# Performance work log

Hardware: AMD Instinct MI355X
Metric: run time of the kernel (lower is better)

## Reference

```python
import jax, jax.numpy as jnp
import numpy as np

N_NODES = 100000


def setup_inputs() -> dict:
    key = jax.random.key(0)
    k1, k2, k3 = jax.random.split(key, 3)
    x = jax.random.normal(k1, (N_NODES, 128), dtype=jnp.float32)
    # Flattened hyperedge membership: src_idx = member node ids, dst_idx = target
    # node id of the owning hyperedge (repeated once per member).
    src_idx = jax.random.randint(k2, (2000000,), 0, N_NODES, dtype=jnp.int64)
    dst_idx = jax.random.randint(k3, (2000000,), 0, N_NODES, dtype=jnp.int64)
    return {"x": x, "src_idx": src_idx, "dst_idx": dst_idx}


def reference(x, src_idx, dst_idx):
    # Gather member features, aggregate per target node, add residual.
    # (The torch identity-stack weight matmul is exactly a per-hyperedge sum,
    #  which the flattened scatter_add reproduces.)
    x_j = x[src_idx]                                        # [E_total, d]
    agg = jax.ops.segment_sum(x_j, dst_idx, num_segments=x.shape[0])  # [N, d]
    return x + agg
```

## Files before the change

kernel.cpp:

```cpp
#include <hip/hip_runtime.h>
#include <hip/hip_fp16.h>


constexpr int DIM = 128;
constexpr int BSHIFT = 7;
constexpr int GNODES = 1 << BSHIFT;
constexpr int MAXB = 1024;
constexpr int CE = 8192;
constexpr int CAP_MAX = 3072;
constexpr int QCAP = 1536;
constexpr int CONVCH = 8192;

__global__ void hgnn_fused_prep(const float4* __restrict__ x4,
                                ushort4* __restrict__ xh4, int n4,
                                const int* __restrict__ src,
                                const int* __restrict__ dst,
                                int* __restrict__ cursor,
                                int* __restrict__ arena, int cap,
                                int* __restrict__ spillCnt,
                                int2* __restrict__ spill, int spillCap,
                                int* __restrict__ qctr, int nChunks,
                                int nedges, int nbk, int nPart) {
    __shared__ int h[MAXB];
    __shared__ int lb[MAXB];
    __shared__ int chunkS;
    const int tid = threadIdx.x;

    if ((int)blockIdx.x < nPart) {
        int c0 = blockIdx.x * CE;
        int c1 = min(c0 + CE, nedges);
        for (int i = tid; i < nbk; i += blockDim.x) h[i] = 0;
        __syncthreads();
        for (int i = c0 + tid; i < c1; i += blockDim.x)
            atomicAdd(&h[dst[i] >> BSHIFT], 1);
        __syncthreads();
        for (int i = tid; i < nbk; i += blockDim.x)
            lb[i] = h[i] ? atomicAdd(&cursor[i], h[i]) : 0;
        __syncthreads();
        for (int i = c0 + tid; i < c1; i += blockDim.x) {
            int s = src[i];
            int d = dst[i];
            int bk = d >> BSHIFT;
            int pos = atomicAdd(&lb[bk], 1);
            if (pos < cap) {
                arena[(size_t)bk * cap + pos] = s | ((d & (GNODES - 1)) << 17);
            } else {
                int sp = atomicAdd(spillCnt, 1);
                if (sp < spillCap) spill[sp] = make_int2(s, d);
            }
        }
    } else if ((int)blockIdx.x == nPart) {
        if (tid < 32) {
            ushort4 z; z.x = 0; z.y = 0; z.z = 0; z.w = 0;
            xh4[n4 + tid] = z;
        }
    }

    for (;;) {
        if (tid == 0) chunkS = atomicAdd(qctr, 1);
        __syncthreads();
        int chunk = chunkS;
        __syncthreads();
        if (chunk >= nChunks) break;
        int i0 = chunk * CONVCH;
        int i1 = min(i0 + CONVCH, n4);
        for (int i = i0 + tid; i < i1; i += blockDim.x) {
            float4 v = x4[i];
            ushort4 o;
            o.x = __half_as_ushort(__float2half_rn(v.x));
            o.y = __half_as_ushort(__float2half_rn(v.y));
            o.z = __half_as_ushort(__float2half_rn(v.z));
            o.w = __half_as_ushort(__float2half_rn(v.w));
            xh4[i] = o;
        }
    }
}

__global__ void hgnn_aggregate(const float4* __restrict__ x4,
                               const uint2* __restrict__ xh,
                               const int* __restrict__ arena, int cap,
                               const int* __restrict__ cursor,
                               float4* __restrict__ out4, int nnodes,
                               int* __restrict__ spillCnt,
                               int2* __restrict__ spill, int spillCap) {
    __shared__ int qsorted[QCAP];
    __shared__ int hoff[33];
    __shared__ int hcur[32];

    const int b = blockIdx.x >> 2;
    const int q = blockIdx.x & 3;
    const int tid = threadIdx.x;
    const int wv = tid >> 6;
    const int lane = tid & 63;
    const int h = lane >> 5;
    const int c = lane & 31;
    const int ZROW = nnodes;

    int cnt = cursor[b];
    if (cnt > cap) cnt = cap;
    const int* ar = arena + (size_t)b * cap;

    if (tid < 32) hcur[tid] = 0;
    __syncthreads();
    for (int i = tid; i < cnt; i += blockDim.x) {
        int dl = ar[i] >> 17;
        if ((dl >> 5) == q) atomicAdd(&hcur[dl & 31], 1);
    }
    __syncthreads();

    int myc = (tid < 32) ? hcur[tid] : 0;
    if (tid < 32) hoff[tid + 1] = myc;
    if (tid == 0) hoff[0] = 0;
    __syncthreads();
    for (int off = 1; off < 32; off <<= 1) {
        int v = (tid < 32 && tid >= off) ? hoff[tid + 1 - off] : 0;
        __syncthreads();
        if (tid < 32) hoff[tid + 1] += v;
        __syncthreads();
    }
    if (tid < 32) hcur[tid] = hoff[tid];
    __syncthreads();

    for (int i = tid; i < cnt; i += blockDim.x) {
        int p = ar[i];
        int dl = p >> 17;
        if ((dl >> 5) == q) {
            int pos = atomicAdd(&hcur[dl & 31], 1);
            if (pos < QCAP) {
                qsorted[pos] = p;
            } else {
                int sp = atomicAdd(spillCnt, 1);
                if (sp < spillCap)
                    spill[sp] = make_int2(p & 0x1FFFF, (b << BSHIFT) + dl);
            }
        }
    }
    __syncthreads();

    const int nodeBase = (b << BSHIFT) + q * 32 + wv * 8;
    const __half2 hz = __floats2half2_rn(0.f, 0.f);
    for (int r = 0; r < 8; r += 2) {
        int n0 = nodeBase + r;
        if (n0 >= nnodes) break;
        int n1 = n0 + 1;
        bool has1 = n1 < nnodes;

        int bin0 = wv * 8 + r;
        int s0 = hoff[bin0];
        int e0 = hoff[bin0 + 1];
        int s1 = hoff[bin0 + 1];
        int e1 = hoff[bin0 + 2];
        if (s0 > QCAP) s0 = QCAP;
        if (e0 > QCAP) e0 = QCAP;
        if (s1 > QCAP) s1 = QCAP;
        if (e1 > QCAP) e1 = QCAP;
        int m0 = e0 - s0;
        int m1 = has1 ? (e1 - s1) : 0;
        int mm = max(m0, m1);

        __half2 a0lo = hz, a0hi = hz, b0lo = hz, b0hi = hz;
        __half2 a1lo = hz, a1hi = hz, b1lo = hz, b1hi = hz;

        for (int j = 0; j < mm; j += 16) {
#pragma unroll
            for (int k = 0; k < 8; ++k) {
                int e = j + 2 * k + h;
                int p0 = (e < m0) ? (qsorted[s0 + e] & 0x1FFFF) : ZROW;
                int p1 = (e < m1) ? (qsorted[s1 + e] & 0x1FFFF) : ZROW;
                uint2 v0 = xh[(size_t)p0 * 32 + c];
                uint2 v1 = xh[(size_t)p1 * 32 + c];
                __half2 v0lo = *reinterpret_cast<const __half2*>(&v0.x);
                __half2 v0hi = *reinterpret_cast<const __half2*>(&v0.y);
                __half2 v1lo = *reinterpret_cast<const __half2*>(&v1.x);
                __half2 v1hi = *reinterpret_cast<const __half2*>(&v1.y);
                if (k & 1) {
                    b0lo = __hadd2(b0lo, v0lo); b0hi = __hadd2(b0hi, v0hi);
                    b1lo = __hadd2(b1lo, v1lo); b1hi = __hadd2(b1hi, v1hi);
                } else {
                    a0lo = __hadd2(a0lo, v0lo); a0hi = __hadd2(a0hi, v0hi);
                    a1lo = __hadd2(a1lo, v1lo); a1hi = __hadd2(a1hi, v1hi);
                }
            }
        }

        {
            __half2 slo = __hadd2(a0lo, b0lo);
            __half2 shi = __hadd2(a0hi, b0hi);
            float2 flo = __half22float2(slo);
            float2 fhi = __half22float2(shi);
            float ax = flo.x + __shfl_xor(flo.x, 32);
            float ay = flo.y + __shfl_xor(flo.y, 32);
            float az = fhi.x + __shfl_xor(fhi.x, 32);
            float aw = fhi.y + __shfl_xor(fhi.y, 32);
            if (h == 0) {
                float4 xv = x4[(size_t)n0 * 32 + c];
                out4[(size_t)n0 * 32 + c] =
                    make_float4(xv.x + ax, xv.y + ay, xv.z + az, xv.w + aw);
            }
        }
        if (has1) {
            __half2 slo = __hadd2(a1lo, b1lo);
            __half2 shi = __hadd2(a1hi, b1hi);
            float2 flo = __half22float2(slo);
            float2 fhi = __half22float2(shi);
            float ax = flo.x + __shfl_xor(flo.x, 32);
            float ay = flo.y + __shfl_xor(flo.y, 32);
            float az = fhi.x + __shfl_xor(fhi.x, 32);
            float aw = fhi.y + __shfl_xor(fhi.y, 32);
            if (h == 0) {
                float4 xv = x4[(size_t)n1 * 32 + c];
                out4[(size_t)n1 * 32 + c] =
                    make_float4(xv.x + ax, xv.y + ay, xv.z + az, xv.w + aw);
            }
        }
    }
}

__global__ void hgnn_spill_apply(const float4* __restrict__ x4,
                                 const int* __restrict__ spillCnt,
                                 const int2* __restrict__ spill,
                                 float* __restrict__ out, int spillCap) {
    int n = *spillCnt;
    if (n > spillCap) n = spillCap;
    int i = blockIdx.x * blockDim.x + threadIdx.x;
    int stride = gridDim.x * blockDim.x;
    for (int k = i; k < n * 32; k += stride) {
        int e = k >> 5;
        int cc = k & 31;
        int2 sd = spill[e];
        float4 v = x4[(size_t)sd.x * 32 + cc];
        float* o = out + (size_t)sd.y * DIM + cc * 4;
        atomicAdd(o + 0, v.x);
        atomicAdd(o + 1, v.y);
        atomicAdd(o + 2, v.z);
        atomicAdd(o + 3, v.w);
    }
}

static inline size_t align256(size_t v) { return (v + 255) & ~(size_t)255; }

extern "C" void kernel_launch(void* const* d_in, const int* in_sizes, int n_in,
                              void* d_out, int out_size, void* d_ws, size_t ws_size,
                              hipStream_t stream) {
    const float* x = (const float*)d_in[0];
    const int* src = (const int*)d_in[1];
    const int* dst = (const int*)d_in[2];
    float* out = (float*)d_out;

    const int E = in_sizes[1];
    const int N = in_sizes[0] / DIM;
    const int n4 = N * (DIM / 4);
    const int NBK = (N + GNODES - 1) >> BSHIFT;
    const int nPart = (E + CE - 1) / CE;
    const int nChunks = (n4 + CONVCH - 1) / CONVCH;

    char* w = (char*)d_ws;
    size_t curBytes = align256((size_t)(MAXB + 2) * sizeof(int));
    size_t xhBytes = align256((size_t)(N + 1) * DIM * 2);
    size_t fixedBytes = curBytes + xhBytes;
    size_t spillReserve = 256 * 1024;

    size_t avail = (ws_size > fixedBytes + spillReserve)
                       ? (ws_size - fixedBytes - spillReserve) : 0;
    int cap = (int)((avail / sizeof(int)) / (size_t)NBK);
    if (cap > CAP_MAX) cap = CAP_MAX;
    if (cap < 64) cap = 64;

    int* cursor = (int*)w;
    int* spillCnt = cursor + MAXB;
    int* qctr = cursor + MAXB + 1;
    ushort* xh = (ushort*)(w + curBytes);
    int* arena = (int*)(w + fixedBytes);
    size_t arenaBytes = align256((size_t)NBK * cap * sizeof(int));
    int2* spill = (int2*)(w + fixedBytes + arenaBytes);
    int spillCap = (int)((ws_size > fixedBytes + arenaBytes)
                             ? (ws_size - fixedBytes - arenaBytes) / sizeof(int2)
                             : 0);

    (void)hipMemsetAsync(cursor, 0, (size_t)(MAXB + 2) * sizeof(int), stream);

    {
        int grid = nPart + 1024;
        hipLaunchKernelGGL(hgnn_fused_prep, dim3(grid), dim3(256), 0, stream,
                           (const float4*)x, (ushort4*)xh, n4,
                           src, dst, cursor, arena, cap,
                           spillCnt, spill, spillCap,
                           qctr, nChunks, E, NBK, nPart);
    }

    hipLaunchKernelGGL(hgnn_aggregate, dim3(NBK * 4), dim3(256), 0, stream,
                       (const float4*)x, (const uint2*)xh, arena, cap,
                       cursor, (float4*)out, N, spillCnt, spill, spillCap);

    hipLaunchKernelGGL(hgnn_spill_apply, dim3(64), dim3(256), 0, stream,
                       (const float4*)x, spillCnt, spill, out, spillCap);
}
```

Measured before the change: 147.6 us.

## Use 16-byte fp16 row gathers with quarter-wave edges and static conversion split

The aggregate kernel now has each 16-lane quarter-wave gather one full fp16 row with uint4 loads, so each wave handles four edges per step instead of two. The two nodes are processed in separate loops, and the partial sums are reduced with two half2 shuffles before the fp32 residual add. The prep kernel drops its atomic work queue for fp32-to-fp16 conversion and uses a static grid-stride loop over more dedicated blocks, which removes the queue counter and its memset slot. Wider loads should cut instruction count and raise bytes per request. The risk is more fp16 rounding from the extra half-precision adds, and conversion blocks that no longer pick up work dynamically after the partition blocks finish.

```diff
diff --git a/kernel.cpp b/kernel.cpp
--- a/kernel.cpp
+++ b/kernel.cpp
@@ -9,7 +9,6 @@
 constexpr int CE = 8192;
 constexpr int CAP_MAX = 3072;
 constexpr int QCAP = 1536;
-constexpr int CONVCH = 8192;
 
 __global__ void hgnn_fused_prep(const float4* __restrict__ x4,
                                 ushort4* __restrict__ xh4, int n4,
@@ -19,11 +18,9 @@
                                 int* __restrict__ arena, int cap,
                                 int* __restrict__ spillCnt,
                                 int2* __restrict__ spill, int spillCap,
-                                int* __restrict__ qctr, int nChunks,
                                 int nedges, int nbk, int nPart) {
     __shared__ int h[MAXB];
     __shared__ int lb[MAXB];
-    __shared__ int chunkS;
     const int tid = threadIdx.x;
 
     if ((int)blockIdx.x < nPart) {
@@ -49,35 +46,29 @@
                 if (sp < spillCap) spill[sp] = make_int2(s, d);
             }
         }
-    } else if ((int)blockIdx.x == nPart) {
-        if (tid < 32) {
-            ushort4 z; z.x = 0; z.y = 0; z.z = 0; z.w = 0;
-            xh4[n4 + tid] = z;
-        }
-    }
-
-    for (;;) {
-        if (tid == 0) chunkS = atomicAdd(qctr, 1);
-        __syncthreads();
-        int chunk = chunkS;
-        __syncthreads();
-        if (chunk >= nChunks) break;
-        int i0 = chunk * CONVCH;
-        int i1 = min(i0 + CONVCH, n4);
-        for (int i = i0 + tid; i < i1; i += blockDim.x) {
-            float4 v = x4[i];
+    } else {
+        int bid = blockIdx.x - nPart;
+        int nconv = gridDim.x - nPart;
+        int i = bid * blockDim.x + tid;
+        int stride = nconv * blockDim.x;
+        for (int k = i; k < n4; k += stride) {
+            float4 v = x4[k];
             ushort4 o;
             o.x = __half_as_ushort(__float2half_rn(v.x));
             o.y = __half_as_ushort(__float2half_rn(v.y));
             o.z = __half_as_ushort(__float2half_rn(v.z));
             o.w = __half_as_ushort(__float2half_rn(v.w));
-            xh4[i] = o;
+            xh4[k] = o;
+        }
+        if (bid == 0 && tid < 32) {
+            ushort4 z; z.x = 0; z.y = 0; z.z = 0; z.w = 0;
+            xh4[n4 + tid] = z;
         }
     }
 }
 
 __global__ void hgnn_aggregate(const float4* __restrict__ x4,
-                               const uint2* __restrict__ xh,
+                               const uint4* __restrict__ xh16,
                                const int* __restrict__ arena, int cap,
                                const int* __restrict__ cursor,
                                float4* __restrict__ out4, int nnodes,
@@ -92,8 +83,8 @@
     const int tid = threadIdx.x;
     const int wv = tid >> 6;
     const int lane = tid & 63;
-    const int h = lane >> 5;
-    const int c = lane & 31;
+    const int qg = lane >> 4;
+    const int cl = lane & 15;
     const int ZROW = nnodes;
 
     int cnt = cursor[b];
@@ -158,59 +149,92 @@
         int m1 = has1 ? (e1 - s1) : 0;
         int mm = max(m0, m1);
 
-        __half2 a0lo = hz, a0hi = hz, b0lo = hz, b0hi = hz;
-        __half2 a1lo = hz, a1hi = hz, b1lo = hz, b1hi = hz;
+        __half2 a0[4] = {hz, hz, hz, hz}, b0[4] = {hz, hz, hz, hz};
+        __half2 a1[4] = {hz, hz, hz, hz}, b1[4] = {hz, hz, hz, hz};
 
         for (int j = 0; j < mm; j += 16) {
 #pragma unroll
-            for (int k = 0; k < 8; ++k) {
-                int e = j + 2 * k + h;
-                int p0 = (e < m0) ? (qsorted[s0 + e] & 0x1FFFF) : ZROW;
-                int p1 = (e < m1) ? (qsorted[s1 + e] & 0x1FFFF) : ZROW;
-                uint2 v0 = xh[(size_t)p0 * 32 + c];
-                uint2 v1 = xh[(size_t)p1 * 32 + c];
-                __half2 v0lo = *reinterpret_cast<const __half2*>(&v0.x);
-                __half2 v0hi = *reinterpret_cast<const __half2*>(&v0.y);
-                __half2 v1lo = *reinterpret_cast<const __half2*>(&v1.x);
-                __half2 v1hi = *reinterpret_cast<const __half2*>(&v1.y);
-                if (k & 1) {
-                    b0lo = __hadd2(b0lo, v0lo); b0hi = __hadd2(b0hi, v0hi);
-                    b1lo = __hadd2(b1lo, v1lo); b1hi = __hadd2(b1hi, v1hi);
+            for (int kk = 0; kk < 4; ++kk) {
+                int e = j + 4 * kk + qg;
+                int p = (e < m0) ? (qsorted[s0 + e] & 0x1FFFF) : ZROW;
+                uint4 v = xh16[(size_t)p * 16 + cl];
+                __half2 h0 = *reinterpret_cast<const __half2*>(&v.x);
+                __half2 h1 = *reinterpret_cast<const __half2*>(&v.y);
+                __half2 h2 = *reinterpret_cast<const __half2*>(&v.z);
+                __half2 h3 = *reinterpret_cast<const __half2*>(&v.w);
+                if (kk & 1) {
+                    b0[0] = __hadd2(b0[0], h0); b0[1] = __hadd2(b0[1], h1);
+                    b0[2] = __hadd2(b0[2], h2); b0[3] = __hadd2(b0[3], h3);
                 } else {
-                    a0lo = __hadd2(a0lo, v0lo); a0hi = __hadd2(a0hi, v0hi);
-                    a1lo = __hadd2(a1lo, v1lo); a1hi = __hadd2(a1hi, v1hi);
+                    a0[0] = __hadd2(a0[0], h0); a0[1] = __hadd2(a0[1], h1);
+                    a0[2] = __hadd2(a0[2], h2); a0[3] = __hadd2(a0[3], h3);
                 }
             }
+#pragma unroll
+            for (int kk = 0; kk < 4; ++kk) {
+                int e = j + 4 * kk + qg;
+                int p = (e < m1) ? (qsorted[s1 + e] & 0x1FFFF) : ZROW;
+                uint4 v = xh16[(size_t)p * 16 + cl];
+                __half2 h0 = *reinterpret_cast<const __half2*>(&v.x);
+                __half2 h1 = *reinterpret_cast<const __half2*>(&v.y);
+                __half2 h2 = *reinterpret_cast<const __half2*>(&v.z);
+                __half2 h3 = *reinterpret_cast<const __half2*>(&v.w);
+                if (kk & 1) {
+                    b1[0] = __hadd2(b1[0], h0); b1[1] = __hadd2(b1[1], h1);
+                    b1[2] = __hadd2(b1[2], h2); b1[3] = __hadd2(b1[3], h3);
+                } else {
+                    a1[0] = __hadd2(a1[0], h0); a1[1] = __hadd2(a1[1], h1);
+                    a1[2] = __hadd2(a1[2], h2); a1[3] = __hadd2(a1[3], h3);
+                }
+            }
         }
 
         {
-            __half2 slo = __hadd2(a0lo, b0lo);
-            __half2 shi = __hadd2(a0hi, b0hi);
-            float2 flo = __half22float2(slo);
-            float2 fhi = __half22float2(shi);
-            float ax = flo.x + __shfl_xor(flo.x, 32);
-            float ay = flo.y + __shfl_xor(flo.y, 32);
-            float az = fhi.x + __shfl_xor(fhi.x, 32);
-            float aw = fhi.y + __shfl_xor(fhi.y, 32);
-            if (h == 0) {
-                float4 xv = x4[(size_t)n0 * 32 + c];
-                out4[(size_t)n0 * 32 + c] =
-                    make_float4(xv.x + ax, xv.y + ay, xv.z + az, xv.w + aw);
+            float f[8];
+#pragma unroll
+            for (int t = 0; t < 4; ++t) {
+                __half2 s = __hadd2(a0[t], b0[t]);
+                int si = *reinterpret_cast<int*>(&s);
+                int sx = __shfl_xor(si, 16);
+                s = __hadd2(s, *reinterpret_cast<__half2*>(&sx));
+                si = *reinterpret_cast<int*>(&s);
+                sx = __shfl_xor(si, 32);
+                s = __hadd2(s, *reinterpret_cast<__half2*>(&sx));
+                float2 fv = __half22float2(s);
+                f[2 * t] = fv.x;
+                f[2 * t + 1] = fv.y;
+            }
+            if (qg == 0) {
+                float4 xa = x4[(size_t)n0 * 32 + 2 * cl];
+                float4 xb = x4[(size_t)n0 * 32 + 2 * cl + 1];
+                out4[(size_t)n0 * 32 + 2 * cl] =
+                    make_float4(xa.x + f[0], xa.y + f[1], xa.z + f[2], xa.w + f[3]);
+                out4[(size_t)n0 * 32 + 2 * cl + 1] =
+                    make_float4(xb.x + f[4], xb.y + f[5], xb.z + f[6], xb.w + f[7]);
             }
         }
         if (has1) {
-            __half2 slo = __hadd2(a1lo, b1lo);
-            __half2 shi = __hadd2(a1hi, b1hi);
-            float2 flo = __half22float2(slo);
-            float2 fhi = __half22float2(shi);
-            float ax = flo.x + __shfl_xor(flo.x, 32);
-            float ay = flo.y + __shfl_xor(flo.y, 32);
-            float az = fhi.x + __shfl_xor(fhi.x, 32);
-            float aw = fhi.y + __shfl_xor(fhi.y, 32);
-            if (h == 0) {
-                float4 xv = x4[(size_t)n1 * 32 + c];
-                out4[(size_t)n1 * 32 + c] =
-                    make_float4(xv.x + ax, xv.y + ay, xv.z + az, xv.w + aw);
+            float f[8];
+#pragma unroll
+            for (int t = 0; t < 4; ++t) {
+                __half2 s = __hadd2(a1[t], b1[t]);
+                int si = *reinterpret_cast<int*>(&s);
+                int sx = __shfl_xor(si, 16);
+                s = __hadd2(s, *reinterpret_cast<__half2*>(&sx));
+                si = *reinterpret_cast<int*>(&s);
+                sx = __shfl_xor(si, 32);
+                s = __hadd2(s, *reinterpret_cast<__half2*>(&sx));
+                float2 fv = __half22float2(s);
+                f[2 * t] = fv.x;
+                f[2 * t + 1] = fv.y;
+            }
+            if (qg == 0) {
+                float4 xa = x4[(size_t)n1 * 32 + 2 * cl];
+                float4 xb = x4[(size_t)n1 * 32 + 2 * cl + 1];
+                out4[(size_t)n1 * 32 + 2 * cl] =
+                    make_float4(xa.x + f[0], xa.y + f[1], xa.z + f[2], xa.w + f[3]);
+                out4[(size_t)n1 * 32 + 2 * cl + 1] =
+                    make_float4(xb.x + f[4], xb.y + f[5], xb.z + f[6], xb.w + f[7]);
             }
         }
     }
@@ -252,10 +276,9 @@
     const int n4 = N * (DIM / 4);
     const int NBK = (N + GNODES - 1) >> BSHIFT;
     const int nPart = (E + CE - 1) / CE;
-    const int nChunks = (n4 + CONVCH - 1) / CONVCH;
 
     char* w = (char*)d_ws;
-    size_t curBytes = align256((size_t)(MAXB + 2) * sizeof(int));
+    size_t curBytes = align256((size_t)(MAXB + 1) * sizeof(int));
     size_t xhBytes = align256((size_t)(N + 1) * DIM * 2);
     size_t fixedBytes = curBytes + xhBytes;
     size_t spillReserve = 256 * 1024;
@@ -268,7 +291,6 @@
 
     int* cursor = (int*)w;
     int* spillCnt = cursor + MAXB;
-    int* qctr = cursor + MAXB + 1;
     ushort* xh = (ushort*)(w + curBytes);
     int* arena = (int*)(w + fixedBytes);
     size_t arenaBytes = align256((size_t)NBK * cap * sizeof(int));
@@ -277,19 +299,18 @@
                              ? (ws_size - fixedBytes - arenaBytes) / sizeof(int2)
                              : 0);
 
-    (void)hipMemsetAsync(cursor, 0, (size_t)(MAXB + 2) * sizeof(int), stream);
+    (void)hipMemsetAsync(cursor, 0, (size_t)(MAXB + 1) * sizeof(int), stream);
 
     {
-        int grid = nPart + 1024;
+        int grid = nPart + 1792;
         hipLaunchKernelGGL(hgnn_fused_prep, dim3(grid), dim3(256), 0, stream,
                            (const float4*)x, (ushort4*)xh, n4,
                            src, dst, cursor, arena, cap,
-                           spillCnt, spill, spillCap,
-                           qctr, nChunks, E, NBK, nPart);
+                           spillCnt, spill, spillCap, E, NBK, nPart);
     }
 
     hipLaunchKernelGGL(hgnn_aggregate, dim3(NBK * 4), dim3(256), 0, stream,
-                       (const float4*)x, (const uint2*)xh, arena, cap,
+                       (const float4*)x, (const uint4*)xh, arena, cap,
                        cursor, (float4*)out, N, spillCnt, spill, spillCap);
 
     hipLaunchKernelGGL(hgnn_spill_apply, dim3(64), dim3(256), 0, stream,
```

After: 141.5 us, median of 2. 1.04x faster.
